# Kernel tuning notes

Measured on AMD Instinct MI355X. Metric: run time of the kernel, lower is better.

Reference implementation:

```python
import jax, jax.numpy as jnp
import numpy as np

IN, HID = 1024, 1024
B, T = 64, 512

def _linear_params(key, fan_in, fan_out):
    # torch nn.Linear default init: U(-1/sqrt(fan_in), 1/sqrt(fan_in))
    k1, k2 = jax.random.split(key)
    bound = 1.0 / np.sqrt(fan_in)
    W = jax.random.uniform(k1, (fan_in, fan_out), minval=-bound, maxval=bound, dtype=jnp.float32)
    b = jax.random.uniform(k2, (fan_out,), minval=-bound, maxval=bound, dtype=jnp.float32)
    return W, b

def setup_inputs() -> dict:
    key = jax.random.key(0)
    keys = jax.random.split(key, 7)
    inputs = jax.random.normal(keys[0], (B, T, IN), dtype=jnp.float32)
    W_ir, b_ir = _linear_params(keys[1], IN, HID)
    W_hr, b_hr = _linear_params(keys[2], HID, HID)
    W_iz, b_iz = _linear_params(keys[3], IN, HID)
    W_hz, b_hz = _linear_params(keys[4], HID, HID)
    W_in, b_in = _linear_params(keys[5], IN, HID)
    W_hn, b_hn = _linear_params(keys[6], HID, HID)
    return dict(inputs=inputs,
                W_ir=W_ir, b_ir=b_ir, W_hr=W_hr, b_hr=b_hr,
                W_iz=W_iz, b_iz=b_iz, W_hz=W_hz, b_hz=b_hz,
                W_in=W_in, b_in=b_in, W_hn=W_hn, b_hn=b_hn)

def reference(inputs, W_ir, b_ir, W_hr, b_hr, W_iz, b_iz, W_hz, b_hz, W_in, b_in, W_hn, b_hn):
    # time-major: [T, B, IN]
    x = jnp.transpose(inputs, (1, 0, 2))
    # precompute input-side projections in one batched GEMM each (same math)
    xr = jnp.einsum('tbi,ih->tbh', x, W_ir) + b_ir
    xz = jnp.einsum('tbi,ih->tbh', x, W_iz) + b_iz
    xn = jnp.einsum('tbi,ih->tbh', x, W_in) + b_in
    h0 = jnp.zeros((1, HID), dtype=inputs.dtype)  # broadcasts over batch like torch

    def step(h, gates):
        gr, gz, gn = gates
        r = jax.nn.sigmoid(gr + h @ W_hr + b_hr)
        z = jax.nn.sigmoid(gz + h @ W_hz + b_hz)
        n = jnp.tanh(gn + r * (h @ W_hn + b_hn))
        h_new = (1.0 - z) * n + z * h
        return h_new, h_new

    h_t, output = jax.lax.scan(step, jnp.broadcast_to(h0, (x.shape[1], HID)), (xr, xz, xn))
    return output, h_t
```

## Files before the change

### kernel.cpp

```cpp
#include <hip/hip_runtime.h>
#include <cstdint>
#include <cstddef>

#define TT   512
#define BATCH 64
#define HID  1024
#define KDIM 1024

typedef short bf16x8 __attribute__((ext_vector_type(8)));
typedef float f32x4 __attribute__((ext_vector_type(4)));

__device__ __forceinline__ unsigned short f2b(float f) {
    unsigned int u = __float_as_uint(f);
    u = (u + 0x7fffu + ((u >> 16) & 1u)) >> 16;
    return (unsigned short)u;
}

__global__ __launch_bounds__(256) void k_init(
    const float* __restrict__ b_ir, const float* __restrict__ b_iz, const float* __restrict__ b_in,
    const float* __restrict__ b_hr, const float* __restrict__ b_hz, const float* __restrict__ b_hn,
    float* __restrict__ bias_x, float* __restrict__ bias_h,
    unsigned short* __restrict__ hbf, int* __restrict__ flags, int* __restrict__ gcnt)
{
    int gid = blockIdx.x * 256 + threadIdx.x;
    if (gid < HID) {
        bias_x[gid]        = b_ir[gid];
        bias_x[HID + gid]  = b_iz[gid];
        bias_x[2*HID + gid]= b_in[gid];
        bias_h[gid]        = b_hr[gid];
        bias_h[HID + gid]  = b_hz[gid];
        bias_h[2*HID + gid]= b_hn[gid];
    }
    ushort4 z4 = make_ushort4(0, 0, 0, 0);
    ushort4* p = reinterpret_cast<ushort4*>(hbf);
    p[2*gid]   = z4;
    p[2*gid+1] = z4;
    if (gid < 256 * 16) flags[gid] = 0;
    if (gid < 16) gcnt[gid] = 0;
}

__global__ __launch_bounds__(256) void k_trans(
    const float* __restrict__ w0, const float* __restrict__ w1, const float* __restrict__ w2,
    const float* __restrict__ w3, const float* __restrict__ w4, const float* __restrict__ w5,
    unsigned short* __restrict__ wxT, unsigned short* __restrict__ whT)
{
    __shared__ float tile[32][33];
    int z = blockIdx.z;
    const float* src = (z == 0) ? w0 : (z == 1) ? w1 : (z == 2) ? w2
                     : (z == 3) ? w3 : (z == 4) ? w4 : w5;
    unsigned short* dst = (z < 3) ? (wxT + (size_t)z * HID * KDIM)
                                  : (whT + (size_t)(z - 3) * HID * KDIM);
    int kb = blockIdx.x * 32, jb = blockIdx.y * 32;
    int tx = threadIdx.x, ty = threadIdx.y;
    #pragma unroll
    for (int p = 0; p < 4; p++)
        tile[tx][ty + 8*p] = src[(size_t)(kb + ty + 8*p) * HID + jb + tx];
    __syncthreads();
    #pragma unroll
    for (int p = 0; p < 4; p++) {
        int n = jb + ty + 8*p;
        dst[(size_t)n * KDIM + kb + tx] = f2b(tile[ty + 8*p][tx]);
    }
}

#define BM 128
#define BN 128
#define LDA 72

__global__ __launch_bounds__(256, 2) void k_gemm_x(
    const float* __restrict__ x,
    const unsigned short* __restrict__ wxT,
    const float* __restrict__ biasx,
    float* __restrict__ ggr, float* __restrict__ ggz, float* __restrict__ ggn)
{
    __shared__ unsigned short lA[BM * LDA];
    __shared__ unsigned short lB[BN * LDA];
    int tid  = threadIdx.x;
    int wave = tid >> 6, lane = tid & 63;
    int l16  = lane & 15, lhi = lane >> 4;
    int rbase = blockIdx.x * BM;
    int nbase = blockIdx.y * BN;
    int wm = (wave >> 1) * 64, wn = (wave & 1) * 64;

    f32x4 acc[4][4];
    for (int a = 0; a < 4; a++)
        for (int b = 0; b < 4; b++)
            acc[a][b] = f32x4{0.f, 0.f, 0.f, 0.f};

    int arow = tid >> 4;
    int acol = (tid & 15) * 4;
    int brow = tid >> 3;
    int bcol = (tid & 7) * 8;

    for (int kb = 0; kb < KDIM; kb += 64) {
        __syncthreads();
        #pragma unroll
        for (int p = 0; p < 8; p++) {
            int r = p * 16 + arow;
            float4 v = *(const float4*)(x + (size_t)(rbase + r) * KDIM + kb + acol);
            ushort4 s;
            s.x = f2b(v.x); s.y = f2b(v.y); s.z = f2b(v.z); s.w = f2b(v.w);
            *(ushort4*)(lA + r * LDA + acol) = s;
        }
        #pragma unroll
        for (int p = 0; p < 4; p++) {
            int r = p * 32 + brow;
            bf16x8 v = *(const bf16x8*)(wxT + (size_t)(nbase + r) * KDIM + kb + bcol);
            *(bf16x8*)(lB + r * LDA + bcol) = v;
        }
        __syncthreads();
        #pragma unroll
        for (int kk = 0; kk < 2; kk++) {
            bf16x8 af[4], bfr[4];
            #pragma unroll
            for (int mt = 0; mt < 4; mt++)
                af[mt] = *(const bf16x8*)(lA + (wm + mt*16 + l16) * LDA + kk*32 + lhi*8);
            #pragma unroll
            for (int nt = 0; nt < 4; nt++)
                bfr[nt] = *(const bf16x8*)(lB + (wn + nt*16 + l16) * LDA + kk*32 + lhi*8);
            #pragma unroll
            for (int mt = 0; mt < 4; mt++)
                #pragma unroll
                for (int nt = 0; nt < 4; nt++)
                    acc[mt][nt] = __builtin_amdgcn_mfma_f32_16x16x32_bf16(
                        af[mt], bfr[nt], acc[mt][nt], 0, 0, 0);
        }
    }
    #pragma unroll
    for (int nt = 0; nt < 4; nt++) {
        int n = nbase + wn + nt*16 + l16;
        float bv = biasx[n];
        int g = n >> 10;
        int j = n & 1023;
        float* outp = (g == 0) ? ggr : (g == 1) ? ggz : ggn;
        #pragma unroll
        for (int mt = 0; mt < 4; mt++) {
            #pragma unroll
            for (int i = 0; i < 4; i++) {
                int R = rbase + wm + mt*16 + lhi*4 + i;
                size_t orow = (size_t)((R & 511) * BATCH + (R >> 9));
                outp[orow * HID + j] = acc[mt][nt][i] + bv;
            }
        }
    }
}

__global__ __launch_bounds__(256, 1) void k_recur(
    const float* __restrict__ ggr, const float* __restrict__ ggz,
    float* __restrict__ dout,
    const unsigned short* __restrict__ whT,
    const float* __restrict__ biash,
    unsigned short* __restrict__ hbf,
    int* __restrict__ flags,
    int* __restrict__ gcnt)
{
    __shared__ f32x4 red[6 * 4 * 64];
    __shared__ unsigned long long hsu[64];
    __shared__ int shr[1];
    unsigned short* hsp = (unsigned short*)hsu;

    int tid  = threadIdx.x;
    if (tid == 0) shr[0] = atomicAdd(gcnt, 1);
    __syncthreads();
    int grank = shr[0];
    int grp   = (grank >> 5) & 7;
    int rank  = grank & 31;

    int w    = tid >> 6, lane = tid & 63;
    int l16  = lane & 15, lhi = lane >> 4;
    int row  = tid >> 5;
    int col  = tid & 31;
    int colbase = rank * 32;
    int b_t  = grp * 8 + row;
    int j_t  = colbase + col;
    int hrow = grp * 8 + (l16 & 7);
    int kbase = w * 256 + lhi * 8;

    bf16x8 wf[2][3][8];
    #pragma unroll
    for (int ct = 0; ct < 2; ct++)
        #pragma unroll
        for (int g = 0; g < 3; g++) {
            const unsigned short* base =
                whT + (size_t)(g * HID + colbase + ct * 16 + l16) * KDIM + kbase;
            #pragma unroll
            for (int kk = 0; kk < 8; kk++)
                wf[ct][g][kk] = *(const bf16x8*)(base + kk * 32);
        }
    #pragma unroll
    for (int ct = 0; ct < 2; ct++)
        #pragma unroll
        for (int g = 0; g < 3; g++)
            #pragma unroll
            for (int kk = 0; kk < 8; kk++)
                asm volatile("" : "+v"(wf[ct][g][kk]));

    float bhr = biash[j_t], bhz = biash[HID + j_t], bhn = biash[2*HID + j_t];

    float hp = 0.f;
    float cgr, cgz, cgn;
    {
        size_t g0 = (size_t)b_t * HID + j_t;
        cgr = ggr[g0]; cgz = ggz[g0]; cgn = dout[g0];
    }

    int* pollp  = flags + (size_t)(grp * 32 + w * 8 + (lane & 7)) * 16;
    int* myflag = flags + (size_t)(grp * 32 + rank) * 16;

    #pragma unroll 1
    for (int t = 0; t < TT; t++) {
        if (t > 0) {
            int guard = 0;
            bool ok;
            do {
                int f = __hip_atomic_load(pollp, __ATOMIC_RELAXED, __HIP_MEMORY_SCOPE_AGENT);
                ok = (f >= t);
            } while (!__all(ok) && ++guard < (1 << 17));
        }

        const unsigned short* hb = hbf + (size_t)(t & 1) * BATCH * HID
                                 + (size_t)hrow * HID + kbase;
        unsigned long long hu[16];
        #pragma unroll
        for (int kk = 0; kk < 8; kk++) {
            hu[2*kk]   = __hip_atomic_load((unsigned long long*)(hb + kk*32),
                                           __ATOMIC_RELAXED, __HIP_MEMORY_SCOPE_AGENT);
            hu[2*kk+1] = __hip_atomic_load((unsigned long long*)(hb + kk*32) + 1,
                                           __ATOMIC_RELAXED, __HIP_MEMORY_SCOPE_AGENT);
        }

        float ngr = 0.f, ngz = 0.f, ngn = 0.f;
        if (t + 1 < TT) {
            size_t g1 = (size_t)((t + 1) * BATCH + b_t) * HID + j_t;
            ngr = ggr[g1]; ngz = ggz[g1]; ngn = dout[g1];
        }

        f32x4 acc[2][3];
        #pragma unroll
        for (int ct = 0; ct < 2; ct++)
            #pragma unroll
            for (int g = 0; g < 3; g++)
                acc[ct][g] = f32x4{0.f, 0.f, 0.f, 0.f};
        #pragma unroll
        for (int kk = 0; kk < 8; kk++) {
            union { unsigned long long u[2]; bf16x8 v; } fa;
            fa.u[0] = hu[2*kk]; fa.u[1] = hu[2*kk+1];
            #pragma unroll
            for (int ct = 0; ct < 2; ct++)
                #pragma unroll
                for (int g = 0; g < 3; g++)
                    acc[ct][g] = __builtin_amdgcn_mfma_f32_16x16x32_bf16(
                        fa.v, wf[ct][g][kk], acc[ct][g], 0, 0, 0);
        }

        #pragma unroll
        for (int ct = 0; ct < 2; ct++)
            #pragma unroll
            for (int g = 0; g < 3; g++)
                red[((g * 2 + ct) * 4 + w) * 64 + lane] = acc[ct][g];
        __syncthreads();
        int ctt = col >> 4, ri = row & 3;
        int lsrc = (row >> 2) * 16 + (col & 15);
        float s0 = 0.f, s1 = 0.f, s2 = 0.f;
        #pragma unroll
        for (int ww = 0; ww < 4; ww++) {
            s0 += red[((0 * 2 + ctt) * 4 + ww) * 64 + lsrc][ri];
            s1 += red[((1 * 2 + ctt) * 4 + ww) * 64 + lsrc][ri];
            s2 += red[((2 * 2 + ctt) * 4 + ww) * 64 + lsrc][ri];
        }

        float r  = 1.f / (1.f + __expf(-(cgr + s0 + bhr)));
        float z  = 1.f / (1.f + __expf(-(cgz + s1 + bhz)));
        float nv = cgn + r * (s2 + bhn);
        float th = 1.f - 2.f / (1.f + __expf(2.f * nv));
        float hv = (1.f - z) * th + z * hp;
        hp = hv;
        dout[((size_t)t * BATCH + b_t) * HID + j_t] = hv;
        if (t == TT - 1) {
            dout[(size_t)TT * BATCH * HID + (size_t)b_t * HID + j_t] = hv;
            break;
        }
        cgr = ngr; cgz = ngz; cgn = ngn;

        hsp[row * 32 + col] = f2b(hv);
        __syncthreads();
        if (tid < 64) {
            int rr = tid >> 3, ch = tid & 7;
            unsigned long long v = hsu[rr * 8 + ch];
            unsigned long long* dst = (unsigned long long*)(
                hbf + (size_t)((t + 1) & 1) * BATCH * HID
                    + (size_t)(grp * 8 + rr) * HID + colbase + ch * 4);
            __hip_atomic_store(dst, v, __ATOMIC_RELAXED, __HIP_MEMORY_SCOPE_AGENT);
            asm volatile("s_waitcnt vmcnt(0)" ::: "memory");
            if (tid == 0)
                __hip_atomic_store(myflag, t + 1,
                                   __ATOMIC_RELAXED, __HIP_MEMORY_SCOPE_AGENT);
        }
    }
}

extern "C" void kernel_launch(void* const* d_in, const int* in_sizes, int n_in,
                              void* d_out, int out_size, void* d_ws, size_t ws_size,
                              hipStream_t stream)
{
    const float* x    = (const float*)d_in[0];
    const float* W_ir = (const float*)d_in[1];
    const float* b_ir = (const float*)d_in[2];
    const float* W_hr = (const float*)d_in[3];
    const float* b_hr = (const float*)d_in[4];
    const float* W_iz = (const float*)d_in[5];
    const float* b_iz = (const float*)d_in[6];
    const float* W_hz = (const float*)d_in[7];
    const float* b_hz = (const float*)d_in[8];
    const float* W_in = (const float*)d_in[9];
    const float* b_in = (const float*)d_in[10];
    const float* W_hn = (const float*)d_in[11];
    const float* b_hn = (const float*)d_in[12];
    float* out = (float*)d_out;

    char* ws = (char*)d_ws;
    size_t off = 0;
    auto alloc = [&](size_t bytes) -> char* {
        char* p = ws + off;
        off += (bytes + 255) & ~(size_t)255;
        return p;
    };
    float*          ggr      = (float*)alloc((size_t)TT * BATCH * HID * 4);
    float*          ggz      = (float*)alloc((size_t)TT * BATCH * HID * 4);
    unsigned short* wxT      = (unsigned short*)alloc((size_t)3 * HID * KDIM * 2);
    unsigned short* whT      = (unsigned short*)alloc((size_t)3 * HID * KDIM * 2);
    float*          bias_x   = (float*)alloc(3 * HID * 4);
    float*          bias_h   = (float*)alloc(3 * HID * 4);
    unsigned short* hbf      = (unsigned short*)alloc((size_t)2 * BATCH * HID * 2);
    int*            flags    = (int*)alloc(256 * 16 * 4);
    int*            gcnt     = (int*)alloc(16 * 4);

    k_init<<<64, 256, 0, stream>>>(b_ir, b_iz, b_in, b_hr, b_hz, b_hn,
                                   bias_x, bias_h, hbf, flags, gcnt);
    k_trans<<<dim3(32, 32, 6), dim3(32, 8), 0, stream>>>(W_ir, W_iz, W_in,
                                                         W_hr, W_hz, W_hn, wxT, whT);
    k_gemm_x<<<dim3(256, 24), 256, 0, stream>>>(x, wxT, bias_x, ggr, ggz, out);
    k_recur<<<256, 256, 0, stream>>>(ggr, ggz, out, whT, bias_h, hbf, flags, gcnt);
}
```

Measured before the change: 2.839 ms.

## Replicate per-block flags so each block polls a private row, move output stores off critical path

The inter-block flag layout changes from one padded flag per producer, polled by all 32 consumers in the group, to a 32x32 matrix per group. Each producer writes its step count into every consumer's private row, so pollers read a contiguous private line instead of contending on shared lines. Hidden-state bf16 values are now written directly from every thread with 2-byte atomic stores instead of being staged through LDS and written as 64-bit chunks. The dout store and the next-step gate prefetch move after the flag publish so they stay off the dependency chain. The cost is 32 flag stores per block per step and many small scattered h stores.

```diff
diff --git a/kernel.cpp b/kernel.cpp
--- a/kernel.cpp
+++ b/kernel.cpp
@@ -20,7 +20,7 @@
     const float* __restrict__ b_ir, const float* __restrict__ b_iz, const float* __restrict__ b_in,
     const float* __restrict__ b_hr, const float* __restrict__ b_hz, const float* __restrict__ b_hn,
     float* __restrict__ bias_x, float* __restrict__ bias_h,
-    unsigned short* __restrict__ hbf, int* __restrict__ flags, int* __restrict__ gcnt)
+    unsigned short* __restrict__ hbf, int* __restrict__ flags2, int* __restrict__ gcnt)
 {
     int gid = blockIdx.x * 256 + threadIdx.x;
     if (gid < HID) {
@@ -35,7 +35,7 @@
     ushort4* p = reinterpret_cast<ushort4*>(hbf);
     p[2*gid]   = z4;
     p[2*gid+1] = z4;
-    if (gid < 256 * 16) flags[gid] = 0;
+    if (gid < 8 * 32 * 32) flags2[gid] = 0;
     if (gid < 16) gcnt[gid] = 0;
 }
 
@@ -151,13 +151,11 @@
     const unsigned short* __restrict__ whT,
     const float* __restrict__ biash,
     unsigned short* __restrict__ hbf,
-    int* __restrict__ flags,
+    int* __restrict__ flags2,
     int* __restrict__ gcnt)
 {
     __shared__ f32x4 red[6 * 4 * 64];
-    __shared__ unsigned long long hsu[64];
     __shared__ int shr[1];
-    unsigned short* hsp = (unsigned short*)hsu;
 
     int tid  = threadIdx.x;
     if (tid == 0) shr[0] = atomicAdd(gcnt, 1);
@@ -204,8 +202,8 @@
         cgr = ggr[g0]; cgz = ggz[g0]; cgn = dout[g0];
     }
 
-    int* pollp  = flags + (size_t)(grp * 32 + w * 8 + (lane & 7)) * 16;
-    int* myflag = flags + (size_t)(grp * 32 + rank) * 16;
+    int* pollp   = flags2 + ((size_t)(grp * 32 + rank) * 32) + w * 8 + (lane & 7);
+    int* flagrow = flags2 + (size_t)grp * 32 * 32;
 
     #pragma unroll 1
     for (int t = 0; t < TT; t++) {
@@ -217,6 +215,7 @@
                 ok = (f >= t);
             } while (!__all(ok) && ++guard < (1 << 17));
         }
+        __builtin_amdgcn_sched_barrier(0);
 
         const unsigned short* hb = hbf + (size_t)(t & 1) * BATCH * HID
                                  + (size_t)hrow * HID + kbase;
@@ -227,12 +226,6 @@
                                            __ATOMIC_RELAXED, __HIP_MEMORY_SCOPE_AGENT);
             hu[2*kk+1] = __hip_atomic_load((unsigned long long*)(hb + kk*32) + 1,
                                            __ATOMIC_RELAXED, __HIP_MEMORY_SCOPE_AGENT);
-        }
-
-        float ngr = 0.f, ngz = 0.f, ngn = 0.f;
-        if (t + 1 < TT) {
-            size_t g1 = (size_t)((t + 1) * BATCH + b_t) * HID + j_t;
-            ngr = ggr[g1]; ngz = ggz[g1]; ngn = dout[g1];
         }
 
         f32x4 acc[2][3];
@@ -275,27 +268,26 @@
         float th = 1.f - 2.f / (1.f + __expf(2.f * nv));
         float hv = (1.f - z) * th + z * hp;
         hp = hv;
-        dout[((size_t)t * BATCH + b_t) * HID + j_t] = hv;
         if (t == TT - 1) {
+            dout[((size_t)t * BATCH + b_t) * HID + j_t] = hv;
             dout[(size_t)TT * BATCH * HID + (size_t)b_t * HID + j_t] = hv;
             break;
         }
-        cgr = ngr; cgz = ngz; cgn = ngn;
-
-        hsp[row * 32 + col] = f2b(hv);
+
+        {
+            unsigned short* hdst = hbf + (size_t)((t + 1) & 1) * BATCH * HID
+                                 + (size_t)b_t * HID + j_t;
+            __hip_atomic_store(hdst, f2b(hv), __ATOMIC_RELAXED, __HIP_MEMORY_SCOPE_AGENT);
+        }
+        asm volatile("s_waitcnt vmcnt(0)" ::: "memory");
         __syncthreads();
-        if (tid < 64) {
-            int rr = tid >> 3, ch = tid & 7;
-            unsigned long long v = hsu[rr * 8 + ch];
-            unsigned long long* dst = (unsigned long long*)(
-                hbf + (size_t)((t + 1) & 1) * BATCH * HID
-                    + (size_t)(grp * 8 + rr) * HID + colbase + ch * 4);
-            __hip_atomic_store(dst, v, __ATOMIC_RELAXED, __HIP_MEMORY_SCOPE_AGENT);
-            asm volatile("s_waitcnt vmcnt(0)" ::: "memory");
-            if (tid == 0)
-                __hip_atomic_store(myflag, t + 1,
-                                   __ATOMIC_RELAXED, __HIP_MEMORY_SCOPE_AGENT);
-        }
+        if (tid < 32)
+            __hip_atomic_store(flagrow + tid * 32 + rank, t + 1,
+                               __ATOMIC_RELAXED, __HIP_MEMORY_SCOPE_AGENT);
+
+        dout[((size_t)t * BATCH + b_t) * HID + j_t] = hv;
+        size_t g1 = (size_t)((t + 1) * BATCH + b_t) * HID + j_t;
+        cgr = ggr[g1]; cgz = ggz[g1]; cgn = dout[g1];
     }
 }
 
@@ -332,13 +324,13 @@
     float*          bias_x   = (float*)alloc(3 * HID * 4);
     float*          bias_h   = (float*)alloc(3 * HID * 4);
     unsigned short* hbf      = (unsigned short*)alloc((size_t)2 * BATCH * HID * 2);
-    int*            flags    = (int*)alloc(256 * 16 * 4);
+    int*            flags2   = (int*)alloc((size_t)8 * 32 * 32 * 4);
     int*            gcnt     = (int*)alloc(16 * 4);
 
     k_init<<<64, 256, 0, stream>>>(b_ir, b_iz, b_in, b_hr, b_hz, b_hn,
-                                   bias_x, bias_h, hbf, flags, gcnt);
+                                   bias_x, bias_h, hbf, flags2, gcnt);
     k_trans<<<dim3(32, 32, 6), dim3(32, 8), 0, stream>>>(W_ir, W_iz, W_in,
                                                          W_hr, W_hz, W_hn, wxT, whT);
     k_gemm_x<<<dim3(256, 24), 256, 0, stream>>>(x, wxT, bias_x, ggr, ggz, out);
-    k_recur<<<256, 256, 0, stream>>>(ggr, ggz, out, whT, bias_h, hbf, flags, gcnt);
-}
+    k_recur<<<256, 256, 0, stream>>>(ggr, ggz, out, whT, bias_h, hbf, flags2, gcnt);
+}
```

New measurement: 2.644 ms. 1.07x faster.
